# Optimization experiments

Measured on AMD Instinct MI355X. Metric: run time of the kernel, lower is better.

## Reference

```python
import jax, jax.numpy as jnp
import numpy as np

D = 64        # d_model
HEADS = 4
DH = D // HEADS   # 16 per-head dim (shared QK)
DEPTH = 4
NHASH = 4
BS = 64       # bucket_size
FF = 4 * D
SELF_ATTN_VAL = -5e4  # reformer-pytorch TOKEN_SELF_ATTN_VALUE


def layer_norm(x, g, b, eps=1e-5):
    m = x.mean(-1, keepdims=True)
    v = ((x - m) ** 2).mean(-1, keepdims=True)
    return (x - m) * jax.lax.rsqrt(v + eps) * g + b


def lsh_attention(x, wqk, wv, wo_w, wo_b, rot):
    # x: (B, L, D); rot: (DH, NHASH, n_buckets//2) fixed random rotations
    B, L, _ = x.shape
    nb = L // BS                       # n_buckets
    qk = x @ wqk                        # shared query/key projection, no bias
    v = x @ wv

    def split_heads(t):
        return t.reshape(B, L, HEADS, DH).transpose(0, 2, 1, 3).reshape(B * HEADS, L, DH)

    qk, v = split_heads(qk), split_heads(v)
    Bh = B * HEADS

    # --- LSH hashing: argmax over [rot, -rot] projections ---
    rotated = jnp.einsum('btf,fhi->bhti', qk, rot)          # (Bh, NHASH, L, nb//2)
    rotated = jnp.concatenate([rotated, -rotated], axis=-1)  # (Bh, NHASH, L, nb)
    buckets = jnp.argmax(rotated, axis=-1)                   # (Bh, NHASH, L)
    offsets = (jnp.arange(NHASH) * nb)[None, :, None]
    buckets = (buckets + offsets).reshape(Bh, NHASH * L)

    # --- sort tokens by (bucket, position) ---
    ticker = jnp.arange(NHASH * L)
    bkt_t = buckets * L + (ticker % L)[None, :]
    sticker = jnp.argsort(bkt_t, axis=-1)
    undo_sort = jnp.argsort(sticker, axis=-1)
    st = sticker % L                                          # (Bh, NHASH*L)

    sqk = jnp.take_along_axis(qk, st[..., None], axis=1)
    sv = jnp.take_along_axis(v, st[..., None], axis=1)

    n_chunks = NHASH * nb
    bq_t = st.reshape(Bh, n_chunks, BS)
    bqk = sqk.reshape(Bh, n_chunks, BS, DH)
    bv = sv.reshape(Bh, n_chunks, BS, DH)
    bq = bqk
    bk = bqk / jnp.maximum(jnp.linalg.norm(bqk, axis=-1, keepdims=True), 1e-12)

    def look_one_back(t):
        return jnp.concatenate([t, jnp.roll(t, 1, axis=1)], axis=2)

    bk = look_one_back(bk)                    # (Bh, n_chunks, 2*BS, DH)
    bv = look_one_back(bv)
    bkv_t = look_one_back(bq_t[..., None])[..., 0]  # (Bh, n_chunks, 2*BS)

    dots = jnp.einsum('bcie,bcje->bcij', bq, bk) * (DH ** -0.5)
    self_mask = bq_t[:, :, :, None] == bkv_t[:, :, None, :]
    dots = jnp.where(self_mask, SELF_ATTN_VAL, dots)

    lse = jax.scipy.special.logsumexp(dots, axis=-1, keepdims=True)
    probs = jnp.exp(dots - lse)
    bo = jnp.einsum('bcij,bcje->bcie', probs, bv)

    so = bo.reshape(Bh, NHASH * L, DH)
    slog = lse.reshape(Bh, NHASH * L)
    o = jnp.take_along_axis(so, undo_sort[..., None], axis=1).reshape(Bh, NHASH, L, DH)
    logits = jnp.take_along_axis(slog, undo_sort, axis=1).reshape(Bh, NHASH, L, 1)

    # combine hash rounds weighted by their softmax normalizers
    w = jnp.exp(logits - jax.scipy.special.logsumexp(logits, axis=1, keepdims=True))
    out = (o * w).sum(axis=1)                 # (Bh, L, DH)
    out = out.reshape(B, HEADS, L, DH).transpose(0, 2, 1, 3).reshape(B, L, D)
    return out @ wo_w + wo_b


def feed_forward(x, w1, b1, w2, b2):
    return jax.nn.gelu(x @ w1 + b1, approximate=False) @ w2 + b2


def setup_inputs() -> dict:
    key = jax.random.key(0)
    ks = jax.random.split(key, 12)
    B = 16
    s = 0.02
    nb = 1280 // BS  # 20 buckets at padded seq len
    return {
        'wave': jax.random.normal(ks[0], (B, 2, 1250), jnp.float32),
        'in_w': jax.random.normal(ks[1], (2, D), jnp.float32) * s,
        'in_b': jnp.zeros((D,), jnp.float32),
        'ln1_g': jnp.ones((DEPTH, D), jnp.float32),
        'ln1_b': jnp.zeros((DEPTH, D), jnp.float32),
        'wqk': jax.random.normal(ks[2], (DEPTH, D, D), jnp.float32) * s,
        'wv': jax.random.normal(ks[3], (DEPTH, D, D), jnp.float32) * s,
        'wo_w': jax.random.normal(ks[4], (DEPTH, D, D), jnp.float32) * s,
        'wo_b': jnp.zeros((DEPTH, D), jnp.float32),
        'rot': jax.random.normal(ks[5], (DEPTH, DH, NHASH, nb // 2), jnp.float32),
        'ln2_g': jnp.ones((DEPTH, D), jnp.float32),
        'ln2_b': jnp.zeros((DEPTH, D), jnp.float32),
        'w1': jax.random.normal(ks[6], (DEPTH, D, FF), jnp.float32) * s,
        'b1': jnp.zeros((DEPTH, FF), jnp.float32),
        'w2': jax.random.normal(ks[7], (DEPTH, FF, D), jnp.float32) * s,
        'b2': jnp.zeros((DEPTH, D), jnp.float32),
        'out_w': jax.random.normal(ks[8], (D, 1), jnp.float32) * s,
        'out_b': jnp.zeros((1,), jnp.float32),
    }


def reference(wave, in_w, in_b, ln1_g, ln1_b, wqk, wv, wo_w, wo_b, rot,
              ln2_g, ln2_b, w1, b1, w2, b2, out_w, out_b):
    x = wave.transpose(0, 2, 1)               # (B, 1250, 2)
    L0 = x.shape[1]
    pad = (-L0) % (BS * 2)                    # pad to multiple of 128 -> 1280
    x = jnp.pad(x, ((0, 0), (0, pad), (0, 0)))
    x = x @ in_w + in_b                       # (B, L, D)

    # reversible sequence: y1 = x1 + attn(LN(x2)); y2 = x2 + ff(LN(y1))
    x1 = x2 = x
    for i in range(DEPTH):
        x1 = x1 + lsh_attention(layer_norm(x2, ln1_g[i], ln1_b[i]),
                                wqk[i], wv[i], wo_w[i], wo_b[i], rot[i])
        x2 = x2 + feed_forward(layer_norm(x1, ln2_g[i], ln2_b[i]),
                               w1[i], b1[i], w2[i], b2[i])
    x = (x1 + x2) * 0.5
    y = (x @ out_w + out_b)[..., 0]
    return y[:, :L0]
```

## Files before the change

### kernel.cpp

```cpp
#include <hip/hip_runtime.h>
#include <math.h>

#define LSEQ 1280
#define L0SEQ 1250
#define DM 64
#define NHEADS 4
#define DHD 16
#define NHASH 4
#define NBUK 20
#define NCHUNK 80
#define FFD 256
#define NBATCH 16
#define NBH 64

#define XSZ (NBATCH*LSEQ*DM)
#define QKSZ (NBH*LSEQ*DHD)
#define OHSZ (NBH*NHASH*LSEQ*DHD)
#define SLSZ (NBH*NHASH*LSEQ)

typedef __attribute__((ext_vector_type(8))) short frag_ab;
typedef __attribute__((ext_vector_type(4))) float frag_c;

union FU4 { uint4 v; frag_ab f; };

__device__ __forceinline__ unsigned rnbf(float x){
    unsigned b = __float_as_uint(x);
    return (b + 0x7fffu + ((b >> 16) & 1u)) >> 16;
}
__device__ __forceinline__ float bf2f(unsigned h){ return __uint_as_float(h << 16); }
__device__ __forceinline__ unsigned rot16(unsigned x){ return (x >> 16) | (x << 16); }
__device__ __forceinline__ uint4 rot16v(uint4 a){
    uint4 r; r.x=rot16(a.x); r.y=rot16(a.y); r.z=rot16(a.z); r.w=rot16(a.w); return r;
}

__device__ __forceinline__ void split3(float x, unsigned& h, unsigned& m, unsigned& l){
    unsigned bx = __float_as_uint(x);
    h = bx >> 16;
    float r = x - __uint_as_float(bx & 0xffff0000u);
    unsigned br = __float_as_uint(r);
    m = br >> 16;
    float r2 = r - __uint_as_float(br & 0xffff0000u);
    l = __float_as_uint(r2) >> 16;
}

__global__ __launch_bounds__(256) void k_init(
    const float* __restrict__ wave, const float* __restrict__ in_w, const float* __restrict__ in_b,
    float* __restrict__ x1, float* __restrict__ x2,
    const float* __restrict__ wo_w, const float* __restrict__ w1,
    const float* __restrict__ w2, unsigned* __restrict__ wsplit)
{
    if (blockIdx.x < 5120) {
        int idx = blockIdx.x * 256 + threadIdx.x;
        int d = idx & 63;
        int t = idx >> 6;
        int b = t / LSEQ;
        int tt = t % LSEQ;
        float v0 = 0.f, v1 = 0.f;
        if (tt < L0SEQ) {
            v0 = wave[(size_t)(b*2+0)*L0SEQ + tt];
            v1 = wave[(size_t)(b*2+1)*L0SEQ + tt];
        }
        float x = v0 * in_w[d] + v1 * in_w[64 + d] + in_b[d];
        x1[idx] = x;
        x2[idx] = x;
    } else {
        int gid = (blockIdx.x - 5120) * 256 + threadIdx.x;
        int l = gid / 36864;
        int r = gid % 36864;
        float src; unsigned* dst; int idx; int stride;
        if (r < 4096) {
            int k = r >> 6, n = r & 63;
            src = wo_w[l*4096 + k*64 + n];
            dst = wsplit + l*8192;
            idx = (((k>>4)*4 + (n>>4))*16 + (n&15))*16 + (k&15);
            stride = 4096;
        } else if (r < 20480) {
            int rr = r - 4096;
            int k = rr >> 8, n = rr & 255;
            src = w1[l*16384 + k*256 + n];
            dst = wsplit + 32768 + l*32768;
            idx = (((k>>4)*16 + (n>>4))*16 + (n&15))*16 + (k&15);
            stride = 16384;
        } else {
            int rr = r - 20480;
            int k = rr >> 6, n = rr & 63;
            src = w2[l*16384 + k*64 + n];
            dst = wsplit + 163840 + l*32768;
            idx = (((k>>4)*4 + (n>>4))*16 + (n&15))*16 + (k&15);
            stride = 16384;
        }
        unsigned h, m, lo;
        split3(src, h, m, lo);
        dst[idx]          = h | (m<<16);
        dst[idx + stride] = lo | (h<<16);
    }
}

__global__ __launch_bounds__(256) void k_qkv(
    const float* __restrict__ x2, const float* __restrict__ g, const float* __restrict__ bta,
    const float* __restrict__ wqk, const float* __restrict__ wv, const float* __restrict__ rot,
    unsigned* __restrict__ qkvs, int* __restrict__ buckets)
{
    __shared__ float xln[16][68];
    __shared__ float qkt[16][68];
    __shared__ float vvt[16][68];
    __shared__ float rots[640];
    int tid = threadIdx.x;
    int b  = blockIdx.x / 80;
    int t0 = (blockIdx.x % 80) * 16;
    int tok = tid >> 4;
    int cg  = tid & 15;
    int c4  = cg * 4;

    for (int i = tid; i < 640; i += 256) rots[i] = rot[i];

    float4 xv4 = *(const float4*)&x2[((size_t)b*LSEQ + t0 + tok)*DM + c4];
    float s = xv4.x + xv4.y + xv4.z + xv4.w;
    float ss = xv4.x*xv4.x + xv4.y*xv4.y + xv4.z*xv4.z + xv4.w*xv4.w;
    s  += __shfl_xor(s,1);  s  += __shfl_xor(s,2);  s  += __shfl_xor(s,4);  s  += __shfl_xor(s,8);
    ss += __shfl_xor(ss,1); ss += __shfl_xor(ss,2); ss += __shfl_xor(ss,4); ss += __shfl_xor(ss,8);
    float m = s * (1.f/64.f);
    float vr = ss * (1.f/64.f) - m*m;
    float rstd = 1.f / sqrtf(vr + 1e-5f);
    {
        float4 g4 = *(const float4*)&g[c4];
        float4 b4 = *(const float4*)&bta[c4];
        float4 o;
        o.x = (xv4.x-m)*rstd*g4.x + b4.x;
        o.y = (xv4.y-m)*rstd*g4.y + b4.y;
        o.z = (xv4.z-m)*rstd*g4.z + b4.z;
        o.w = (xv4.w-m)*rstd*g4.w + b4.w;
        *(float4*)&xln[tok][c4] = o;
    }
    __syncthreads();

    float aq[4] = {0,0,0,0}, av[4] = {0,0,0,0};
    for (int f = 0; f < 64; f++) {
        float4 wq4 = *(const float4*)&wqk[f*64 + c4];
        float4 wv4 = *(const float4*)&wv [f*64 + c4];
        float xv = xln[tok][f];
        aq[0] += xv*wq4.x; aq[1] += xv*wq4.y; aq[2] += xv*wq4.z; aq[3] += xv*wq4.w;
        av[0] += xv*wv4.x; av[1] += xv*wv4.y; av[2] += xv*wv4.z; av[3] += xv*wv4.w;
    }
    *(float4*)&qkt[tok][c4] = *(float4*)aq;
    *(float4*)&vvt[tok][c4] = *(float4*)av;
    __syncthreads();

    int p = tid >> 2;
    int ptok = p >> 2, head = p & 3;
    int sub = tid & 3;
    int e0 = sub * 4;
    int t = t0 + ptok;
    float4 qf4 = *(const float4*)&qkt[ptok][head*16 + e0];
    float nsq = qf4.x*qf4.x + qf4.y*qf4.y + qf4.z*qf4.z + qf4.w*qf4.w;
    nsq += __shfl_xor(nsq,1); nsq += __shfl_xor(nsq,2);
    float inv = 1.f / fmaxf(sqrtf(nsq), 1e-12f);
    float qe[4] = {qf4.x, qf4.y, qf4.z, qf4.w};
    unsigned wq[4], wk[4];
    #pragma unroll
    for (int i=0;i<4;i++){
        float xq = qe[i]*0.25f;
        unsigned qh = rnbf(xq);
        unsigned ql = rnbf(xq - bf2f(qh));
        wq[i] = qh | (ql<<16);
        float xk = qe[i]*inv;
        unsigned kh = rnbf(xk);
        unsigned kl = rnbf(xk - bf2f(kh));
        wk[i] = kh | (kl<<16);
    }
    float4 vf4 = *(const float4*)&vvt[ptok][head*16 + e0];
    float ve[4] = {vf4.x, vf4.y, vf4.z, vf4.w};
    unsigned wv1[4], wv3[4];
    #pragma unroll
    for (int i=0;i<4;i++){
        unsigned vh_, vm_, vl_;
        split3(ve[i], vh_, vm_, vl_);
        wv1[i] = vh_ | (vm_<<16);
        wv3[i] = vl_ | (vh_<<16);
    }
    size_t sb = (((size_t)(b*NHEADS+head))*LSEQ + t)*64;
    *(uint4*)&qkvs[sb + e0]      = *(uint4*)wq;
    *(uint4*)&qkvs[sb + 16 + e0] = *(uint4*)wk;
    *(uint4*)&qkvs[sb + 32 + e0] = *(uint4*)wv1;
    *(uint4*)&qkvs[sb + 48 + e0] = *(uint4*)wv3;

    float qf[16];
    {
        float4 a0 = *(const float4*)&qkt[ptok][head*16 + 0];
        float4 a1 = *(const float4*)&qkt[ptok][head*16 + 4];
        float4 a2 = *(const float4*)&qkt[ptok][head*16 + 8];
        float4 a3 = *(const float4*)&qkt[ptok][head*16 + 12];
        qf[0]=a0.x; qf[1]=a0.y; qf[2]=a0.z; qf[3]=a0.w;
        qf[4]=a1.x; qf[5]=a1.y; qf[6]=a1.z; qf[7]=a1.w;
        qf[8]=a2.x; qf[9]=a2.y; qf[10]=a2.z; qf[11]=a2.w;
        qf[12]=a3.x; qf[13]=a3.y; qf[14]=a3.z; qf[15]=a3.w;
    }
    int nh = sub;
    float rv[10];
    #pragma unroll
    for (int i=0;i<10;i++) {
        float acc = 0.f;
        #pragma unroll
        for (int f=0; f<16; f++) acc += qf[f]*rots[(f*NHASH+nh)*10 + i];
        rv[i] = acc;
    }
    float best = rv[0]; int bi = 0;
    #pragma unroll
    for (int i=1;i<10;i++) if (rv[i] > best) { best = rv[i]; bi = i; }
    #pragma unroll
    for (int i=0;i<10;i++) if (-rv[i] > best) { best = -rv[i]; bi = 10+i; }
    buckets[((size_t)(b*NHEADS+head)*NHASH + nh)*LSEQ + t] = bi;
}

__global__ __launch_bounds__(256) void k_sort(
    const int* __restrict__ buckets, int* __restrict__ sorted)
{
    __shared__ unsigned long long masks[20][20];
    __shared__ int pre[20][20];
    __shared__ int startl[20];
    int tid = threadIdx.x;
    int w = tid >> 6, lane = tid & 63;
    int gidx = blockIdx.x;
    const int* bk = buckets + (size_t)gidx * LSEQ;
    int* dst = sorted + (size_t)gidx * LSEQ;

    int myb[5];
    #pragma unroll
    for (int i = 0; i < 5; i++) {
        int ch = w*5 + i;
        int bv = bk[ch*64 + lane];
        myb[i] = bv;
        #pragma unroll
        for (int b2 = 0; b2 < 20; b2++) {
            unsigned long long m2 = __ballot(bv == b2);
            if (lane == b2) masks[ch][b2] = m2;
        }
    }
    __syncthreads();
    if (tid < 20) {
        int run = 0;
        for (int ch = 0; ch < 20; ch++) {
            pre[ch][tid] = run;
            run += __popcll(masks[ch][tid]);
        }
        startl[tid] = run;
    }
    __syncthreads();
    if (tid == 0) {
        int acc = 0;
        for (int b2 = 0; b2 < 20; b2++) { int t = startl[b2]; startl[b2] = acc; acc += t; }
    }
    __syncthreads();
    unsigned long long below = (lane == 63) ? 0x7fffffffffffffffull
                                            : ((1ull << lane) - 1ull);
    #pragma unroll
    for (int i = 0; i < 5; i++) {
        int ch = w*5 + i;
        int bv = myb[i];
        int rank = startl[bv] + pre[ch][bv] + __popcll(masks[ch][bv] & below);
        dst[rank] = ch*64 + lane;
    }
}

__global__ __launch_bounds__(256) void k_attn(
    const unsigned* __restrict__ qkvs,
    const int* __restrict__ sorted, float* __restrict__ o_hash, float* __restrict__ slog)
{
    __shared__ __align__(16) unsigned SM[7904];
    unsigned* Va1 = SM;
    unsigned* Ka1 = SM + 2624;
    unsigned* Pa1 = SM + 2624;
    unsigned short* Vlh  = (unsigned short*)(SM + 5184);
    unsigned short* Pa2h = (unsigned short*)(SM + 6496);
    int* kposS = (int*)(SM + 7776);

    int tid = threadIdx.x;
    int bh = blockIdx.x & 63;
    int c  = blockIdx.x >> 6;
    int h  = c / NBUK, cc = c % NBUK;
    int cp = (c + NCHUNK - 1) % NCHUNK;
    int hp = cp / NBUK, ccp = cp % NBUK;

    int key = tid & 127;
    int pos = (key < 64)
        ? sorted[((size_t)bh*NHASH + h)*LSEQ + cc*64 + key]
        : sorted[((size_t)bh*NHASH + hp)*LSEQ + ccp*64 + (key-64)];
    size_t srow = ((size_t)bh*LSEQ + pos)*64;
    if (tid < 128) {
        kposS[key] = pos;
        const uint4* kr = (const uint4*)(qkvs + srow + 16);
        #pragma unroll
        for (int e4=0; e4<4; e4++)
            *(uint4*)&Ka1[key*20 + e4*4] = kr[e4];
    } else {
        const uint4* v1r = (const uint4*)(qkvs + srow + 32);
        const uint4* v3r = (const uint4*)(qkvs + srow + 48);
        int kt = key >> 4, jl = key & 15;
        int lb = kt*328 + jl;
        #pragma unroll
        for (int e4=0; e4<4; e4++){
            uint4 a = v1r[e4], c2 = v3r[e4];
            unsigned aa[4] = {a.x,a.y,a.z,a.w};
            unsigned cb[4] = {c2.x,c2.y,c2.z,c2.w};
            #pragma unroll
            for (int i=0;i<4;i++){
                int d = e4*4 + i;
                Va1[lb + d*20] = aa[i];
                Vlh[lb + d*20] = (unsigned short)(cb[i] & 0xffffu);
            }
        }
    }
    __syncthreads();

    int w = tid >> 6, lane = tid & 63;
    int quad = lane >> 4, col = lane & 15;

    int qgpos = kposS[16*w + col];
    FU4 QA;
    QA.v = *(const uint4*)(qkvs + ((size_t)bh*LSEQ + qgpos)*64 + quad*4);
    frag_ab qA = QA.f;

    frag_c acc[8];
    #pragma unroll
    for (int nt=0; nt<8; nt++){
        FU4 B1, B2;
        B1.v = *(const uint4*)&Ka1[(nt*16+col)*20 + 4*quad];
        B2.v = rot16v(B1.v);
        frag_c a = {0.f,0.f,0.f,0.f};
        a = __builtin_amdgcn_mfma_f32_16x16x32_bf16(qA, B1.f, a, 0, 0, 0);
        a = __builtin_amdgcn_mfma_f32_16x16x32_bf16(qA, B2.f, a, 0, 0, 0);
        acc[nt] = a;
    }
    int qp[4];
    #pragma unroll
    for (int reg=0; reg<4; reg++) qp[reg] = kposS[16*w + quad*4 + reg];
    #pragma unroll
    for (int nt=0; nt<8; nt++){
        int kp2 = kposS[nt*16 + col];
        #pragma unroll
        for (int reg=0; reg<4; reg++)
            if (kp2 == qp[reg]) acc[nt][reg] = -5e4f;
    }
    float mx[4] = {-3.4e38f,-3.4e38f,-3.4e38f,-3.4e38f};
    #pragma unroll
    for (int nt=0; nt<8; nt++)
        #pragma unroll
        for (int reg=0; reg<4; reg++) mx[reg] = fmaxf(mx[reg], acc[nt][reg]);
    #pragma unroll
    for (int reg=0; reg<4; reg++){
        float m2 = mx[reg];
        m2 = fmaxf(m2, __shfl_xor(m2, 1)); m2 = fmaxf(m2, __shfl_xor(m2, 2));
        m2 = fmaxf(m2, __shfl_xor(m2, 4)); m2 = fmaxf(m2, __shfl_xor(m2, 8));
        mx[reg] = m2;
    }
    float sm2[4] = {0.f,0.f,0.f,0.f};
    #pragma unroll
    for (int nt=0; nt<8; nt++)
        #pragma unroll
        for (int reg=0; reg<4; reg++){
            float e = __expf(acc[nt][reg] - mx[reg]);
            acc[nt][reg] = e; sm2[reg] += e;
        }
    #pragma unroll
    for (int reg=0; reg<4; reg++){
        float s2 = sm2[reg];
        s2 += __shfl_xor(s2, 1); s2 += __shfl_xor(s2, 2);
        s2 += __shfl_xor(s2, 4); s2 += __shfl_xor(s2, 8);
        sm2[reg] = s2;
    }
    float invs[4];
    #pragma unroll
    for (int reg=0; reg<4; reg++) invs[reg] = 1.f / sm2[reg];
    if (col == 0) {
        #pragma unroll
        for (int reg=0; reg<4; reg++)
            slog[((size_t)bh*NHASH + h)*LSEQ + qp[reg]] = mx[reg] + __logf(sm2[reg]);
    }

    frag_c o = {0.f,0.f,0.f,0.f};
    __syncthreads();
    #pragma unroll
    for (int pass=0; pass<4; pass++){
        #pragma unroll
        for (int t2=0; t2<2; t2++){
            int nt = pass*2 + t2;
            #pragma unroll
            for (int reg=0; reg<4; reg++){
                float p = acc[nt][reg] * invs[reg];
                unsigned ph_, pm_, pl_;
                split3(p, ph_, pm_, pl_);
                int idx = t2*1280 + (16*w + 4*quad + reg)*20 + col;
                Pa1[idx] = ph_ | (pm_<<16);
                Pa2h[idx] = (unsigned short)pl_;
            }
        }
        __syncthreads();
        #pragma unroll
        for (int t2=0; t2<2; t2++){
            int ktg = pass*2 + t2;
            FU4 A1, A2, B1, B2, B3;
            int pidx = t2*1280 + (16*w + col)*20 + 4*quad;
            A1.v = *(const uint4*)&Pa1[pidx];
            uint2 z = *(const uint2*)&Pa2h[pidx];
            A2.v.x = (A1.v.x & 0xffffu) | (z.x << 16);
            A2.v.y = (A1.v.y & 0xffffu) | (z.x & 0xffff0000u);
            A2.v.z = (A1.v.z & 0xffffu) | (z.y << 16);
            A2.v.w = (A1.v.w & 0xffffu) | (z.y & 0xffff0000u);
            int vidx = ktg*328 + col*20 + 4*quad;
            B1.v = *(const uint4*)&Va1[vidx];
            B2.v = rot16v(B1.v);
            uint2 zl = *(const uint2*)&Vlh[vidx];
            B3.v.x = (zl.x & 0xffffu) | (B1.v.x << 16);
            B3.v.y = (zl.x >> 16)     | (B1.v.y << 16);
            B3.v.z = (zl.y & 0xffffu) | (B1.v.z << 16);
            B3.v.w = (zl.y >> 16)     | (B1.v.w << 16);
            o = __builtin_amdgcn_mfma_f32_16x16x32_bf16(A1.f, B1.f, o, 0, 0, 0);
            o = __builtin_amdgcn_mfma_f32_16x16x32_bf16(A1.f, B2.f, o, 0, 0, 0);
            o = __builtin_amdgcn_mfma_f32_16x16x32_bf16(A2.f, B3.f, o, 0, 0, 0);
        }
        if (pass < 3) __syncthreads();
    }
    size_t obase = ((size_t)bh*NHASH + h)*LSEQ;
    #pragma unroll
    for (int reg=0; reg<4; reg++)
        o_hash[(obase + qp[reg])*DHD + col] = o[reg];
}

__global__ __launch_bounds__(256) void k_tail(
    const float* __restrict__ o_hash, const float* __restrict__ slog,
    const unsigned* __restrict__ wo_s, const float* __restrict__ wo_b,
    const float* __restrict__ g2, const float* __restrict__ b2t,
    const unsigned* __restrict__ w1_s, const float* __restrict__ b1,
    const unsigned* __restrict__ w2_s, const float* __restrict__ b2f,
    float* __restrict__ x1, float* __restrict__ x2,
    const float* __restrict__ out_w, const float* __restrict__ out_b,
    float* __restrict__ y, int do_out)
{
    __shared__ unsigned cA1[1024], cA2[1024];
    __shared__ unsigned xA1[1024], xA2[1024];
    __shared__ unsigned gA1[4096], gA2[4096];
    __shared__ float lnS[64], lnQ[64];
    float* red = (float*)gA1;

    int tid = threadIdx.x;
    int b  = blockIdx.x / 80;
    int t0 = (blockIdx.x % 80) * 16;
    int w = tid >> 6, lane = tid & 63;
    int quad = lane >> 4, col = lane & 15;

    {
        int tok = tid >> 4;
        int dg  = tid & 15;
        int d0  = dg * 4;
        int kt  = dg >> 2;
        int t = t0 + tok;
        int bh = b*NHEADS + kt;
        float sl[4];
        #pragma unroll
        for (int nh=0; nh<4; nh++) sl[nh] = slog[((size_t)bh*NHASH + nh)*LSEQ + t];
        float mx = fmaxf(fmaxf(sl[0],sl[1]), fmaxf(sl[2],sl[3]));
        float wgt[4]; float wsum = 0.f;
        #pragma unroll
        for (int nh=0; nh<4; nh++){ wgt[nh] = __expf(sl[nh]-mx); wsum += wgt[nh]; }
        float iv = 1.f/wsum;
        float a4[4] = {0.f,0.f,0.f,0.f};
        #pragma unroll
        for (int nh=0; nh<4; nh++){
            float4 oh = *(const float4*)&o_hash[(((size_t)bh*NHASH + nh)*LSEQ + t)*DHD + (d0 & 15)];
            float wn = wgt[nh]*iv;
            a4[0] += wn*oh.x; a4[1] += wn*oh.y; a4[2] += wn*oh.z; a4[3] += wn*oh.w;
        }
        int sw = (tok & 7) << 2;
        unsigned cw1[4], cw2[4];
        #pragma unroll
        for (int i=0;i<4;i++){
            unsigned h_, m_, l_;
            split3(a4[i], h_, m_, l_);
            cw1[i] = h_ | (m_<<16);
            cw2[i] = h_ | (l_<<16);
        }
        *(uint4*)&cA1[tok*64 + (d0 ^ sw)] = *(uint4*)cw1;
        *(uint4*)&cA2[tok*64 + (d0 ^ sw)] = *(uint4*)cw2;
    }
    __syncthreads();
    FU4 aA1[4], aA2[4];
    {
        int sw = (col & 7) << 2;
        #pragma unroll
        for (int kt=0; kt<4; kt++){
            int word = (kt*16 + quad*4) ^ sw;
            aA1[kt].v = *(const uint4*)&cA1[col*64 + word];
            aA2[kt].v = *(const uint4*)&cA2[col*64 + word];
        }
    }

    frag_c awo = {0.f,0.f,0.f,0.f};
    #pragma unroll
    for (int kt=0; kt<4; kt++){
        FU4 B1, B2, B3;
        int bidx = ((kt*4 + w)*16 + col)*16 + quad*4;
        B1.v = *(const uint4*)&wo_s[bidx];
        B2.v = rot16v(B1.v);
        B3.v = *(const uint4*)&wo_s[bidx + 4096];
        awo = __builtin_amdgcn_mfma_f32_16x16x32_bf16(aA1[kt].f, B1.f, awo, 0, 0, 0);
        awo = __builtin_amdgcn_mfma_f32_16x16x32_bf16(aA1[kt].f, B2.f, awo, 0, 0, 0);
        awo = __builtin_amdgcn_mfma_f32_16x16x32_bf16(aA2[kt].f, B3.f, awo, 0, 0, 0);
    }
    int cg = w*16 + col;
    float x1n[4];
    float s1[4], s2[4];
    {
        float wb = wo_b[cg];
        #pragma unroll
        for (int reg=0; reg<4; reg++){
            int rg = t0 + quad*4 + reg;
            size_t xi = ((size_t)b*LSEQ + rg)*DM + cg;
            float xv = x1[xi] + awo[reg] + wb;
            x1[xi] = xv;
            x1n[reg] = xv;
            s1[reg] = xv; s2[reg] = xv*xv;
        }
    }
    #pragma unroll
    for (int reg=0; reg<4; reg++){
        float a = s1[reg], q = s2[reg];
        a += __shfl_xor(a,1); a += __shfl_xor(a,2); a += __shfl_xor(a,4); a += __shfl_xor(a,8);
        q += __shfl_xor(q,1); q += __shfl_xor(q,2); q += __shfl_xor(q,4); q += __shfl_xor(q,8);
        s1[reg] = a; s2[reg] = q;
    }
    if (col == 0) {
        #pragma unroll
        for (int reg=0; reg<4; reg++){
            lnS[w*16 + quad*4 + reg] = s1[reg];
            lnQ[w*16 + quad*4 + reg] = s2[reg];
        }
    }
    __syncthreads();
    float mean[4], rstd[4];
    #pragma unroll
    for (int reg=0; reg<4; reg++){
        int tok = quad*4 + reg;
        float a = lnS[tok] + lnS[16+tok] + lnS[32+tok] + lnS[48+tok];
        float q = lnQ[tok] + lnQ[16+tok] + lnQ[32+tok] + lnQ[48+tok];
        mean[reg] = a*(1.f/64.f);
        float var = q*(1.f/64.f) - mean[reg]*mean[reg];
        rstd[reg] = 1.f/sqrtf(var + 1e-5f);
    }
    {
        float gv = g2[cg], bv = b2t[cg];
        #pragma unroll
        for (int reg=0; reg<4; reg++){
            int row = quad*4 + reg;
            float xv = (x1n[reg]-mean[reg])*rstd[reg]*gv + bv;
            unsigned h_, m_, l_;
            split3(xv, h_, m_, l_);
            int word = cg ^ ((row & 7) << 2);
            xA1[row*64 + word] = h_ | (m_<<16);
            xA2[row*64 + word] = h_ | (l_<<16);
        }
    }
    __syncthreads();
    FU4 xa1[4], xa2[4];
    {
        int sw = (col & 7) << 2;
        #pragma unroll
        for (int kt=0; kt<4; kt++){
            int word = (kt*16 + quad*4) ^ sw;
            xa1[kt].v = *(const uint4*)&xA1[col*64 + word];
            xa2[kt].v = *(const uint4*)&xA2[col*64 + word];
        }
    }

    unsigned* myg1 = gA1 + w*1024;
    unsigned* myg2 = gA2 + w*1024;
    #pragma unroll
    for (int ntl=0; ntl<4; ntl++){
        int nt = w*4 + ntl;
        frag_c a = {0.f,0.f,0.f,0.f};
        #pragma unroll
        for (int kt=0; kt<4; kt++){
            FU4 B1, B2, B3;
            int bidx = ((kt*16 + nt)*16 + col)*16 + quad*4;
            B1.v = *(const uint4*)&w1_s[bidx];
            B2.v = rot16v(B1.v);
            B3.v = *(const uint4*)&w1_s[bidx + 16384];
            a = __builtin_amdgcn_mfma_f32_16x16x32_bf16(xa1[kt].f, B1.f, a, 0, 0, 0);
            a = __builtin_amdgcn_mfma_f32_16x16x32_bf16(xa1[kt].f, B2.f, a, 0, 0, 0);
            a = __builtin_amdgcn_mfma_f32_16x16x32_bf16(xa2[kt].f, B3.f, a, 0, 0, 0);
        }
        float bb = b1[nt*16 + col];
        #pragma unroll
        for (int reg=0; reg<4; reg++){
            float xx = a[reg] + bb;
            float ge = 0.5f*xx*(1.f + erff(xx*0.70710678118654752f));
            unsigned h_, m_, l_;
            split3(ge, h_, m_, l_);
            int row = quad*4 + reg;
            int word = (ntl*16 + col) ^ ((row & 7) << 2);
            myg1[row*64 + word] = h_ | (m_<<16);
            myg2[row*64 + word] = h_ | (l_<<16);
        }
    }
    frag_c aw2[4] = {{0,0,0,0},{0,0,0,0},{0,0,0,0},{0,0,0,0}};
    {
        int sw = (col & 7) << 2;
        #pragma unroll
        for (int kt2=0; kt2<4; kt2++){
            FU4 A1, A2;
            int word = (kt2*16 + quad*4) ^ sw;
            A1.v = *(const uint4*)&myg1[col*64 + word];
            A2.v = *(const uint4*)&myg2[col*64 + word];
            int kg = w*4 + kt2;
            #pragma unroll
            for (int nt2=0; nt2<4; nt2++){
                FU4 B1, B2, B3;
                int bidx = ((kg*4 + nt2)*16 + col)*16 + quad*4;
                B1.v = *(const uint4*)&w2_s[bidx];
                B2.v = rot16v(B1.v);
                B3.v = *(const uint4*)&w2_s[bidx + 16384];
                aw2[nt2] = __builtin_amdgcn_mfma_f32_16x16x32_bf16(A1.f, B1.f, aw2[nt2], 0, 0, 0);
                aw2[nt2] = __builtin_amdgcn_mfma_f32_16x16x32_bf16(A1.f, B2.f, aw2[nt2], 0, 0, 0);
                aw2[nt2] = __builtin_amdgcn_mfma_f32_16x16x32_bf16(A2.f, B3.f, aw2[nt2], 0, 0, 0);
            }
        }
    }
    __syncthreads();
    #pragma unroll
    for (int nt2=0; nt2<4; nt2++)
        #pragma unroll
        for (int reg=0; reg<4; reg++)
            red[((w*4 + nt2)*4 + reg)*64 + lane] = aw2[nt2][reg];
    __syncthreads();
    float x2f[4];
    {
        float bb = b2f[cg];
        #pragma unroll
        for (int reg=0; reg<4; reg++){
            float v = red[((0*4 + w)*4 + reg)*64 + lane]
                    + red[((1*4 + w)*4 + reg)*64 + lane]
                    + red[((2*4 + w)*4 + reg)*64 + lane]
                    + red[((3*4 + w)*4 + reg)*64 + lane];
            int rg = t0 + quad*4 + reg;
            size_t xi = ((size_t)b*LSEQ + rg)*DM + cg;
            float nv = x2[xi] + v + bb;
            x2[xi] = nv;
            x2f[reg] = nv;
        }
    }
    if (do_out) {
        float ow = out_w[cg];
        float part[4];
        #pragma unroll
        for (int reg=0; reg<4; reg++){
            float p = (x1n[reg] + x2f[reg]) * 0.5f * ow;
            p += __shfl_xor(p,1); p += __shfl_xor(p,2); p += __shfl_xor(p,4); p += __shfl_xor(p,8);
            part[reg] = p;
        }
        __syncthreads();
        if (col == 0) {
            #pragma unroll
            for (int reg=0; reg<4; reg++)
                lnS[w*16 + quad*4 + reg] = part[reg];
        }
        __syncthreads();
        if (tid < 16) {
            int t = t0 + tid;
            if (t < L0SEQ) {
                float v2 = lnS[tid] + lnS[16+tid] + lnS[32+tid] + lnS[48+tid];
                y[(size_t)b*L0SEQ + t] = v2 + out_b[0];
            }
        }
    }
}

extern "C" void kernel_launch(void* const* d_in, const int* in_sizes, int n_in,
                              void* d_out, int out_size, void* d_ws, size_t ws_size,
                              hipStream_t stream)
{
    const float* wave  = (const float*)d_in[0];
    const float* in_w  = (const float*)d_in[1];
    const float* in_b  = (const float*)d_in[2];
    const float* ln1_g = (const float*)d_in[3];
    const float* ln1_b = (const float*)d_in[4];
    const float* wqk   = (const float*)d_in[5];
    const float* wv    = (const float*)d_in[6];
    const float* wo_w  = (const float*)d_in[7];
    const float* wo_b  = (const float*)d_in[8];
    const float* rot   = (const float*)d_in[9];
    const float* ln2_g = (const float*)d_in[10];
    const float* ln2_b = (const float*)d_in[11];
    const float* w1    = (const float*)d_in[12];
    const float* b1    = (const float*)d_in[13];
    const float* w2    = (const float*)d_in[14];
    const float* b2    = (const float*)d_in[15];
    const float* out_w = (const float*)d_in[16];
    const float* out_b = (const float*)d_in[17];
    float* y = (float*)d_out;

    float* ws = (float*)d_ws;
    float* x1      = ws;
    float* x2      = x1 + XSZ;
    unsigned* qkvs = (unsigned*)(x2 + XSZ);
    float* o_hash  = (float*)(qkvs + 4*QKSZ);
    float* slogb   = o_hash + OHSZ;
    int* buckets   = (int*)(slogb + SLSZ);
    int* sorted    = buckets + SLSZ;
    unsigned* wsplit = (unsigned*)(sorted + SLSZ);

    k_init<<<5696, 256, 0, stream>>>(wave, in_w, in_b, x1, x2, wo_w, w1, w2, wsplit);
    for (int layer = 0; layer < 4; layer++) {
        k_qkv<<<NBATCH*80, 256, 0, stream>>>(x2, ln1_g + layer*64, ln1_b + layer*64,
                                       wqk + layer*4096, wv + layer*4096, rot + layer*640,
                                       qkvs, buckets);
        k_sort<<<256, 256, 0, stream>>>(buckets, sorted);
        k_attn<<<NBH*NCHUNK, 256, 0, stream>>>(qkvs, sorted, o_hash, slogb);
        k_tail<<<NBATCH*LSEQ/16, 256, 0, stream>>>(o_hash, slogb,
                                        wsplit + layer*8192, wo_b + layer*64,
                                        ln2_g + layer*64, ln2_b + layer*64,
                                        wsplit + 32768 + layer*32768, b1 + layer*256,
                                        wsplit + 163840 + layer*32768, b2 + layer*64,
                                        x1, x2,
                                        out_w, out_b, y, (layer == 3) ? 1 : 0);
    }
}
```

Before: 525.9 us.

## Simplify attention P split, defer softmax normalization, and restrict self-mask checks

Within the attention kernel, the probability matrix is now split into only high and mid bf16 parts instead of three, which drops the low-part shared buffer and its extra loads. Softmax normalization moves to the output store: the matrix-multiply inputs use the unnormalized exponentials, and the result is scaled by a fast reciprocal. The self-attention mask now uses the diagonal position of the current chunk, with key-position comparisons kept only for the look-back half when cc==0. Byte-permute instructions replace shift/mask packing. Together these cut LDS traffic, ALU work and shared-memory use, with some loss of precision in P·V.

```diff
diff --git a/kernel.cpp b/kernel.cpp
--- a/kernel.cpp
+++ b/kernel.cpp
@@ -41,6 +41,12 @@
     m = br >> 16;
     float r2 = r - __uint_as_float(br & 0xffff0000u);
     l = __float_as_uint(r2) >> 16;
+}
+
+__device__ __forceinline__ unsigned pack_hm(float x){
+    unsigned bx = __float_as_uint(x);
+    float r = x - __uint_as_float(bx & 0xffff0000u);
+    return __builtin_amdgcn_perm(__float_as_uint(r), bx, 0x07060302u);
 }
 
 __global__ __launch_bounds__(256) void k_init(
@@ -266,13 +272,12 @@
     const unsigned* __restrict__ qkvs,
     const int* __restrict__ sorted, float* __restrict__ o_hash, float* __restrict__ slog)
 {
-    __shared__ __align__(16) unsigned SM[7904];
+    __shared__ __align__(16) unsigned SM[6624];
     unsigned* Va1 = SM;
     unsigned* Ka1 = SM + 2624;
     unsigned* Pa1 = SM + 2624;
     unsigned short* Vlh  = (unsigned short*)(SM + 5184);
-    unsigned short* Pa2h = (unsigned short*)(SM + 6496);
-    int* kposS = (int*)(SM + 7776);
+    int* kposS = (int*)(SM + 6496);
 
     int tid = threadIdx.x;
     int bh = blockIdx.x & 63;
@@ -334,13 +339,23 @@
     int qp[4];
     #pragma unroll
     for (int reg=0; reg<4; reg++) qp[reg] = kposS[16*w + quad*4 + reg];
-    #pragma unroll
-    for (int nt=0; nt<8; nt++){
-        int kp2 = kposS[nt*16 + col];
+
+    #pragma unroll
+    for (int nt=0; nt<8; nt++) if (nt == w) {
         #pragma unroll
         for (int reg=0; reg<4; reg++)
-            if (kp2 == qp[reg]) acc[nt][reg] = -5e4f;
-    }
+            acc[nt][reg] = (col == quad*4 + reg) ? -5e4f : acc[nt][reg];
+    }
+    if (cc == 0) {
+        #pragma unroll
+        for (int nt=4; nt<8; nt++){
+            int kp2 = kposS[nt*16 + col];
+            #pragma unroll
+            for (int reg=0; reg<4; reg++)
+                if (kp2 == qp[reg]) acc[nt][reg] = -5e4f;
+        }
+    }
+
     float mx[4] = {-3.4e38f,-3.4e38f,-3.4e38f,-3.4e38f};
     #pragma unroll
     for (int nt=0; nt<8; nt++)
@@ -370,7 +385,7 @@
     }
     float invs[4];
     #pragma unroll
-    for (int reg=0; reg<4; reg++) invs[reg] = 1.f / sm2[reg];
+    for (int reg=0; reg<4; reg++) invs[reg] = __builtin_amdgcn_rcpf(sm2[reg]);
     if (col == 0) {
         #pragma unroll
         for (int reg=0; reg<4; reg++)
@@ -386,12 +401,8 @@
             int nt = pass*2 + t2;
             #pragma unroll
             for (int reg=0; reg<4; reg++){
-                float p = acc[nt][reg] * invs[reg];
-                unsigned ph_, pm_, pl_;
-                split3(p, ph_, pm_, pl_);
                 int idx = t2*1280 + (16*w + 4*quad + reg)*20 + col;
-                Pa1[idx] = ph_ | (pm_<<16);
-                Pa2h[idx] = (unsigned short)pl_;
+                Pa1[idx] = pack_hm(acc[nt][reg]);
             }
         }
         __syncthreads();
@@ -401,19 +412,18 @@
             FU4 A1, A2, B1, B2, B3;
             int pidx = t2*1280 + (16*w + col)*20 + 4*quad;
             A1.v = *(const uint4*)&Pa1[pidx];
-            uint2 z = *(const uint2*)&Pa2h[pidx];
-            A2.v.x = (A1.v.x & 0xffffu) | (z.x << 16);
-            A2.v.y = (A1.v.y & 0xffffu) | (z.x & 0xffff0000u);
-            A2.v.z = (A1.v.z & 0xffffu) | (z.y << 16);
-            A2.v.w = (A1.v.w & 0xffffu) | (z.y & 0xffff0000u);
+            A2.v.x = A1.v.x & 0xffffu;
+            A2.v.y = A1.v.y & 0xffffu;
+            A2.v.z = A1.v.z & 0xffffu;
+            A2.v.w = A1.v.w & 0xffffu;
             int vidx = ktg*328 + col*20 + 4*quad;
             B1.v = *(const uint4*)&Va1[vidx];
             B2.v = rot16v(B1.v);
             uint2 zl = *(const uint2*)&Vlh[vidx];
-            B3.v.x = (zl.x & 0xffffu) | (B1.v.x << 16);
-            B3.v.y = (zl.x >> 16)     | (B1.v.y << 16);
-            B3.v.z = (zl.y & 0xffffu) | (B1.v.z << 16);
-            B3.v.w = (zl.y >> 16)     | (B1.v.w << 16);
+            B3.v.x = __builtin_amdgcn_perm(B1.v.x, zl.x, 0x05040100u);
+            B3.v.y = __builtin_amdgcn_perm(B1.v.y, zl.x, 0x05040302u);
+            B3.v.z = __builtin_amdgcn_perm(B1.v.z, zl.y, 0x05040100u);
+            B3.v.w = __builtin_amdgcn_perm(B1.v.w, zl.y, 0x05040302u);
             o = __builtin_amdgcn_mfma_f32_16x16x32_bf16(A1.f, B1.f, o, 0, 0, 0);
             o = __builtin_amdgcn_mfma_f32_16x16x32_bf16(A1.f, B2.f, o, 0, 0, 0);
             o = __builtin_amdgcn_mfma_f32_16x16x32_bf16(A2.f, B3.f, o, 0, 0, 0);
@@ -423,7 +433,7 @@
     size_t obase = ((size_t)bh*NHASH + h)*LSEQ;
     #pragma unroll
     for (int reg=0; reg<4; reg++)
-        o_hash[(obase + qp[reg])*DHD + col] = o[reg];
+        o_hash[(obase + qp[reg])*DHD + col] = o[reg] * invs[reg];
 }
 
 __global__ __launch_bounds__(256) void k_tail(
```

Measured after the change: 508.3 us. 3.3% less time.
